# Performance work log

Measured on AMD Instinct MI355X. Metric: run time of the kernel, lower is better.

## Reference

```python
import jax, jax.numpy as jnp
import numpy as np

RATE = 0.75
B, L, D = 4, 4096, 1024
NUM_DROP = int(RATE * L)      # 3072
NUM_KEEP = L - NUM_DROP       # 1024


def setup_inputs() -> dict:
    key = jax.random.key(0)
    k1, k2, k3 = jax.random.split(key, 3)
    inputs = jax.random.normal(k1, (B, L, D), dtype=jnp.float32)
    mask_embedding = 0.02 * jax.random.normal(k2, (D,), dtype=jnp.float32)
    # choice without replacement, then sort (as in the module)
    idx_keep = jnp.sort(jax.random.permutation(k3, L)[:NUM_KEEP]).astype(jnp.int32)
    return {"inputs": inputs, "mask_embedding": mask_embedding, "idx_keep": idx_keep}


def reference(inputs, mask_embedding, idx_keep):
    length = inputs.shape[-2]
    iota = jnp.arange(length, dtype=jnp.int32)

    # index_to_mask / mask_to_index
    mask_keep = jnp.zeros((length,), dtype=jnp.int32).at[idx_keep].set(1)
    mask_drop = 1 - mask_keep
    idx_drop = jnp.nonzero(mask_drop, size=NUM_DROP)[0].astype(jnp.int32)

    dt = inputs.dtype
    # SPMD one-hot matmul gather: [num_keep, length] @ [B, length, D]
    onehot_keep = (idx_keep[:, None] == iota[None, :]).astype(dt)
    outputs_dropped = jnp.einsum('kl,bld->bkd', onehot_keep, inputs)

    # SPMD one-hot matmul scatter of the broadcast mask embedding
    me = mask_embedding.astype(dt)
    updates = jnp.tile(me, (NUM_DROP, 1))                      # [num_drop, D]
    onehot_drop = (idx_drop[:, None] == iota[None, :]).astype(dt)
    scattered = jnp.einsum('nl,nd->ld', onehot_drop, updates)  # [length, D]
    outputs_masked = inputs * mask_keep.astype(dt)[:, None] + scattered

    return (outputs_dropped, outputs_masked, mask_drop.astype(jnp.float32), idx_keep)
```

## Files before the change

### kernel.cpp

```cpp
#include <hip/hip_runtime.h>


#define B_ 4
#define L_ 4096
#define D_ 1024
#define NKEEP_ 1024

__global__ __launch_bounds__(256) void masktoken_kernel(
    const float4* __restrict__ in,
    const float4* __restrict__ me,
    const int*    __restrict__ idx_keep,
    float4* __restrict__ out0,
    float4* __restrict__ out1,
    float*  __restrict__ out2,
    float*  __restrict__ out3)
{
    const int row = blockIdx.x;
    const int b   = row >> 12;
    const int l   = row & (L_ - 1);
    const int t   = threadIdx.x;

    int lo = 0, hi = NKEEP_;
    #pragma unroll
    for (int i = 0; i < 10; ++i) {
        int mid = (lo + hi) >> 1;
        if (idx_keep[mid] < l) lo = mid + 1; else hi = mid;
    }
    const int r = (lo < NKEEP_ && idx_keep[lo] == l) ? lo : -1;

    const size_t rowOff = (size_t)row * (D_ / 4);
    if (r >= 0) {
        float4 v = in[rowOff + t];
        out1[rowOff + t] = v;
        out0[((size_t)b * NKEEP_ + (size_t)r) * (D_ / 4) + t] = v;
    } else {
        out1[rowOff + t] = me[t];
    }

    if (b == 0 && t == 0) {
        out2[l] = (r < 0) ? 1.0f : 0.0f;
        if (r >= 0) out3[r] = (float)l;
    }
}

extern "C" void kernel_launch(void* const* d_in, const int* in_sizes, int n_in,
                              void* d_out, int out_size, void* d_ws, size_t ws_size,
                              hipStream_t stream) {
    const float4* in  = (const float4*)d_in[0];
    const float4* me  = (const float4*)d_in[1];
    const int*    idx = (const int*)d_in[2];

    float* out = (float*)d_out;
    float4* out0 = (float4*)out;
    float4* out1 = (float4*)(out + (size_t)B_ * NKEEP_ * D_);
    float*  out2 = out + (size_t)B_ * NKEEP_ * D_ + (size_t)B_ * L_ * D_;
    float*  out3 = out2 + L_;

    dim3 grid(B_ * L_);
    dim3 block(256);
    masktoken_kernel<<<grid, block, 0, stream>>>(in, me, idx, out0, out1, out2, out3);
}
```

Baseline: 130.1 us.

## Process all batches per row block and use nontemporal loads and stores

Each block now handles one sequence position across all four batches, so the binary search over idx_keep runs once per position instead of once per (batch, position), and the grid shrinks by 4x. Global loads and stores now use nontemporal builtins to avoid cache pollution on this streaming copy. The trade-off is fewer blocks with more memory work each, which may lower the number of loads in flight early on.

Result: no change. 132.3 us (+1.7%).

```diff
diff --git a/kernel.cpp b/kernel.cpp
--- a/kernel.cpp
+++ b/kernel.cpp
@@ -5,20 +5,21 @@
 #define L_ 4096
 #define D_ 1024
 #define NKEEP_ 1024
+#define D4_ (D_ / 4)
+
+typedef float v4f __attribute__((ext_vector_type(4)));
 
 __global__ __launch_bounds__(256) void masktoken_kernel(
-    const float4* __restrict__ in,
-    const float4* __restrict__ me,
-    const int*    __restrict__ idx_keep,
-    float4* __restrict__ out0,
-    float4* __restrict__ out1,
-    float*  __restrict__ out2,
-    float*  __restrict__ out3)
+    const v4f* __restrict__ in,
+    const v4f* __restrict__ me,
+    const int* __restrict__ idx_keep,
+    v4f*   __restrict__ out0,
+    v4f*   __restrict__ out1,
+    float* __restrict__ out2,
+    float* __restrict__ out3)
 {
-    const int row = blockIdx.x;
-    const int b   = row >> 12;
-    const int l   = row & (L_ - 1);
-    const int t   = threadIdx.x;
+    const int l = blockIdx.x;
+    const int t = threadIdx.x;
 
     int lo = 0, hi = NKEEP_;
     #pragma unroll
@@ -28,35 +29,42 @@
     }
     const int r = (lo < NKEEP_ && idx_keep[lo] == l) ? lo : -1;
 
-    const size_t rowOff = (size_t)row * (D_ / 4);
-    if (r >= 0) {
-        float4 v = in[rowOff + t];
-        out1[rowOff + t] = v;
-        out0[((size_t)b * NKEEP_ + (size_t)r) * (D_ / 4) + t] = v;
-    } else {
-        out1[rowOff + t] = me[t];
+    if (t == 0) {
+        out2[l] = (r < 0) ? 1.0f : 0.0f;
+        if (r >= 0) out3[r] = (float)l;
     }
 
-    if (b == 0 && t == 0) {
-        out2[l] = (r < 0) ? 1.0f : 0.0f;
-        if (r >= 0) out3[r] = (float)l;
+    if (r >= 0) {
+        #pragma unroll
+        for (int b = 0; b < B_; ++b) {
+            const size_t src = ((size_t)b * L_ + (size_t)l) * D4_ + t;
+            v4f v = __builtin_nontemporal_load(&in[src]);
+            __builtin_nontemporal_store(v, &out1[src]);
+            __builtin_nontemporal_store(v, &out0[((size_t)b * NKEEP_ + (size_t)r) * D4_ + t]);
+        }
+    } else {
+        const v4f m = me[t];
+        #pragma unroll
+        for (int b = 0; b < B_; ++b) {
+            __builtin_nontemporal_store(m, &out1[((size_t)b * L_ + (size_t)l) * D4_ + t]);
+        }
     }
 }
 
 extern "C" void kernel_launch(void* const* d_in, const int* in_sizes, int n_in,
                               void* d_out, int out_size, void* d_ws, size_t ws_size,
                               hipStream_t stream) {
-    const float4* in  = (const float4*)d_in[0];
-    const float4* me  = (const float4*)d_in[1];
-    const int*    idx = (const int*)d_in[2];
+    const v4f* in  = (const v4f*)d_in[0];
+    const v4f* me  = (const v4f*)d_in[1];
+    const int* idx = (const int*)d_in[2];
 
     float* out = (float*)d_out;
-    float4* out0 = (float4*)out;
-    float4* out1 = (float4*)(out + (size_t)B_ * NKEEP_ * D_);
-    float*  out2 = out + (size_t)B_ * NKEEP_ * D_ + (size_t)B_ * L_ * D_;
-    float*  out3 = out2 + L_;
+    v4f*   out0 = (v4f*)out;
+    v4f*   out1 = (v4f*)(out + (size_t)B_ * NKEEP_ * D_);
+    float* out2 = out + (size_t)B_ * NKEEP_ * D_ + (size_t)B_ * L_ * D_;
+    float* out3 = out2 + L_;
 
-    dim3 grid(B_ * L_);
+    dim3 grid(L_);
     dim3 block(256);
     masktoken_kernel<<<grid, block, 0, stream>>>(in, me, idx, out0, out1, out2, out3);
 }
```
